# Performance work log

Measured on AMD Instinct MI355X. Metric: run time of the kernel, lower is better.

## Reference

```python
import jax, jax.numpy as jnp
import numpy as np

BATCH = 8192
IN_DIM = 512
OUT_DIM = 512
GRID_SIZE = 5
SPLINE_ORDER = 3
# grid has 2*(G+K)+1 knots -> after K de Boor steps basis count = 2*G+K
N_BASES = 2 * GRID_SIZE + SPLINE_ORDER  # 13
CLAMP_EPS = 1e-4
DENOM_EPS = 1e-8


def _make_grid():
    step = 2.0 / GRID_SIZE
    g = jnp.arange(-GRID_SIZE - SPLINE_ORDER, GRID_SIZE + SPLINE_ORDER + 1, dtype=jnp.float32) * step
    return jnp.tile(g[None, :], (IN_DIM, 1))  # [in_dim, 2*(G+K)+1]


def _b_spline(x, grid):
    # x: [B, in], grid: [in, L] -> bases: [B, in, 2*G+K]
    xg = x[..., None]  # [B, in, 1]
    bases = ((xg >= grid[:, :-1]) & (xg < grid[:, 1:])).astype(x.dtype)
    for k in range(1, SPLINE_ORDER + 1):
        denom1 = grid[:, k:-1] - grid[:, :-(k + 1)] + DENOM_EPS
        left = (xg - grid[:, :-(k + 1)]) / denom1
        denom2 = grid[:, k + 1:] - grid[:, 1:-k] + DENOM_EPS
        right = (grid[:, k + 1:] - xg) / denom2
        bases = left * bases[..., :-1] + right * bases[..., 1:]
    return bases


def setup_inputs() -> dict:
    key = jax.random.key(0)
    k1, k2, k3 = jax.random.split(key, 3)
    x = jax.random.normal(k1, (BATCH, IN_DIM), dtype=jnp.float32)
    # kaiming_uniform(a=sqrt(5)) ~ U(-1/sqrt(fan_in), 1/sqrt(fan_in))
    b_c = 1.0 / np.sqrt(IN_DIM * N_BASES)
    coeffs = jax.random.uniform(k2, (OUT_DIM, IN_DIM, N_BASES), dtype=jnp.float32, minval=-b_c, maxval=b_c)
    b_w = 1.0 / np.sqrt(IN_DIM)
    base_weight = jax.random.uniform(k3, (OUT_DIM, IN_DIM), dtype=jnp.float32, minval=-b_w, maxval=b_w)
    return {"x": x, "coeffs": coeffs, "base_weight": base_weight}


def reference(x, coeffs, base_weight):
    grid = _make_grid()
    xc = jnp.clip(x, -1.0 + CLAMP_EPS, 1.0 - CLAMP_EPS)
    basis = _b_spline(xc, grid)                       # [B, in, nb]
    spline_out = jnp.einsum('oic,bic->bo', coeffs, basis)
    base_out = jax.nn.silu(x) @ base_weight.T         # F.linear(silu(x), W)
    y = spline_out + base_out + x                     # residual (in_dim == out_dim)
    return y
```

## Files before the change

### kernel.cpp

```cpp
#include <hip/hip_runtime.h>
#include <stdint.h>

typedef unsigned int u32;
typedef unsigned short u16;
typedef unsigned long long u64;
typedef __bf16 bf16x8 __attribute__((ext_vector_type(8)));
typedef float f32x4 __attribute__((ext_vector_type(4)));
typedef u32 u32x4 __attribute__((ext_vector_type(4)));

#define IN_DIM 512

__device__ __forceinline__ u16 bfr(float f) {
  __bf16 h = (__bf16)f;
  return __builtin_bit_cast(u16, h);
}
__device__ __forceinline__ u16 f2bf(float f) {
  u32 u = __builtin_bit_cast(u32, f);
  u += 0x7fffu + ((u >> 16) & 1u);
  return (u16)(u >> 16);
}
__device__ __forceinline__ u32 pk2(float a, float b) {
  return (u32)f2bf(a) | ((u32)f2bf(b) << 16);
}

__global__ void pack_b(const float* __restrict__ coeffs,
                       const float* __restrict__ bw,
                       char* __restrict__ Bp) {
  __shared__ float stage[64][56];
  const int tid = threadIdx.x;
  const int q = tid & 3, g = tid >> 2;
  const int id = blockIdx.x * 64 + g;
  const int col = id >> 7, s = id & 127;
  const float* cbase = coeffs + ((size_t)col * IN_DIM + s * 4) * 13;
#pragma unroll
  for (int j = 0; j < 3; ++j) {
    int ch = q + j * 4;
    float4 v = *(const float4*)(cbase + ch * 4);
    stage[g][ch * 4 + 0] = v.x; stage[g][ch * 4 + 1] = v.y;
    stage[g][ch * 4 + 2] = v.z; stage[g][ch * 4 + 3] = v.w;
  }
  if (q == 0) {
    float4 v = *(const float4*)(cbase + 48);
    stage[g][48] = v.x; stage[g][49] = v.y; stage[g][50] = v.z; stage[g][51] = v.w;
  }
  if (q == 1) {
    float4 v = *(const float4*)(bw + (size_t)col * IN_DIM + s * 4);
    stage[g][52] = v.x; stage[g][53] = v.y; stage[g][54] = v.z; stage[g][55] = v.w;
  }
  __syncthreads();
  const int nbp = col >> 7, cb = (col >> 4) & 7, cl = col & 15;
  char* base = Bp + (((size_t)(nbp * 128 + s) * 8 + cb) * 2) * 1024;
#pragma unroll
  for (int r = 0; r < 2; ++r) {
    int idx = q * 2 + r;
    int h = idx & 1;
    int dd = idx >> 1;
    int ks = dd >> 1;
    const float* sf = &stage[g][dd * 13];
    float w = stage[g][52 + dd];
    u16 hh[8];
#pragma unroll
    for (int c = 0; c < 8; ++c) {
      int slot = h * 8 + c;
      float v = slot < 13 ? sf[slot] : (slot < 15 ? w : 0.0f);
      hh[c] = bfr(v);
    }
    u32x4 o;
    o.x = (u32)hh[0] | ((u32)hh[1] << 16);
    o.y = (u32)hh[2] | ((u32)hh[3] << 16);
    o.z = (u32)hh[4] | ((u32)hh[5] << 16);
    o.w = (u32)hh[6] | ((u32)hh[7] << 16);
    int lanei = cl + 16 * (2 * (dd & 1) + h);
    *(u32x4*)(base + (size_t)ks * 1024 + lanei * 16) = o;
  }
}

__device__ __forceinline__ void expandA(float xv, char* rb, u32 swz, u32 k0) {
  float xc = fminf(fmaxf(xv, -0.9999f), 0.9999f);
  float tp = __fmaf_rn(xc, 2.5f, 3.0f);
  float fj = floorf(tp);
  int jl = (int)fj;
  float u = tp - fj;
  float u2 = u * u, u3 = u2 * u;
  float vv = 1.0f - u;
  float b0 = vv * vv * vv * (1.0f / 6.0f);
  float b3 = u3 * (1.0f / 6.0f);
  float b1 = __fmaf_rn(0.5f, u3, __fmaf_rn(u2, -1.0f, 2.0f / 3.0f));
  float b2 = 1.0f - b0 - b1 - b3;
  float e = __expf(-xv);
  float sg = __fdividef(xv, 1.0f + e);
  u16 sh = bfr(sg);
  float shf = __builtin_bit_cast(float, ((u32)sh) << 16);
  u16 sl = bfr(sg - shf);
  u32 pk01 = (u32)bfr(b0) | ((u32)bfr(b1) << 16);
  u32 pk23 = (u32)bfr(b2) | ((u32)bfr(b3) << 16);
  u64 v = (u64)pk01 | (((u64)pk23) << 32);
  int sstart = jl + 2;
  int qa = sstart >> 2;
  int shn = (sstart & 3) << 4;
  u64 lo = v << shn;
  u64 hi = shn ? (v >> (64 - shn)) : 0ull;
  u64 q0 = qa ? 0ull : lo;
  u64 q1 = qa ? lo : hi;
  u64 q2 = qa ? hi : 0ull;
  u64 q3 = (u64)(((u32)sh) << 16) | (((u64)(u32)sl) << 32);
  u32x4 c0, c1;
  c0.x = (u32)q0; c0.y = (u32)(q0 >> 32); c0.z = (u32)q1; c0.w = (u32)(q1 >> 32);
  c1.x = (u32)q2; c1.y = (u32)(q2 >> 32); c1.z = (u32)q3; c1.w = (u32)(q3 >> 32);
  *(u32x4*)(rb + ((k0 ^ swz) << 4)) = c0;
  *(u32x4*)(rb + (((k0 + 1u) ^ swz) << 4)) = c1;
}

__launch_bounds__(768, 3)
__global__ void kan_gemm(const float* __restrict__ x,
                         const char* __restrict__ Bp,
                         float* __restrict__ out) {
  __shared__ __align__(16) char smem[67584];

  const int tid = threadIdx.x;
  const int lane = tid & 63;
  const int wid = tid >> 6;
  const bool isC = (wid < 8);

  const int kt = wid >> 2;
  const int wm = (wid >> 1) & 1, wn = wid & 1;
  const int lrow = lane & 15, lkg = lane >> 4;

  int s0 = blockIdx.x;
  int xcd = s0 & 7;
  int nb = xcd >> 1;
  int mb = ((s0 >> 3) << 1) | (xcd & 1);

  const int te = tid & 255;
  const int erow = te >> 2;
  const int ad = te & 3;
  const u32 aswz = (u32)(erow & 7);
  const u32 ak0 = (u32)(ad * 2);
  const float* xpa = x + (size_t)(mb * 128 + erow) * IN_DIM + ad;
  const float* xpb = xpa + (size_t)64 * IN_DIM;

  const char* bptr = Bp + (((size_t)(nb * 128) * 8 + wn * 4) * 2 + kt) * 1024 + (size_t)lane * 16;

  f32x4 acc[4][4];
#pragma unroll
  for (int i = 0; i < 4; ++i)
#pragma unroll
    for (int j = 0; j < 4; ++j) acc[i][j] = (f32x4){0.f, 0.f, 0.f, 0.f};

  u32x4 bA[4], bB[4];
  u32x4 afA[4], afB[4];
  char* r0 = smem;
  char* r1 = smem + 16384;
  char* r2 = smem + 32768;

  float xa1 = 0.f, xa2 = 0.f, xb1 = 0.f, xb2 = 0.f;
  if (isC) {
#pragma unroll
    for (int fn = 0; fn < 4; ++fn)
      bA[fn] = *(const u32x4*)(bptr + fn * 2048);
  } else {
    expandA(xpa[0], r0 + erow * 128, aswz, ak0);
    expandA(xpb[0], r0 + (erow + 64) * 128, aswz, ak0);
    expandA(xpa[4], r1 + erow * 128, aswz, ak0);
    expandA(xpb[4], r1 + (erow + 64) * 128, aswz, ak0);
    xa1 = xpa[8];  xb1 = xpb[8];
    xa2 = xpa[12]; xb2 = xpb[12];
  }
  __syncthreads();

  const u32 asl = (((u32)(kt * 4) | (u32)lkg) ^ (u32)(lrow & 7)) << 4;

  if (isC) {
    const char* arb0 = r0 + (wm * 64 + lrow) * 128;
#pragma unroll
    for (int fm = 0; fm < 4; ++fm)
      afA[fm] = *(const u32x4*)(arb0 + fm * 2048 + asl);
  }

#define STEP(S, RBN, WB, BCUR, BNXT, AFC, AFN)                                 \
  {                                                                            \
    if (isC) {                                                                 \
      const char* arbn = (RBN) + (wm * 64 + lrow) * 128;                       \
      _Pragma("unroll")                                                        \
      for (int fm = 0; fm < 4; ++fm)                                           \
        AFN[fm] = *(const u32x4*)(arbn + fm * 2048 + asl);                     \
      int sl_ = (S) + 1 < 128 ? (S) + 1 : 127;                                 \
      _Pragma("unroll")                                                        \
      for (int fn = 0; fn < 4; ++fn)                                           \
        BNXT[fn] = *(const u32x4*)(bptr + (size_t)sl_ * 16384 + fn * 2048);    \
      __builtin_amdgcn_s_setprio(1);                                           \
      _Pragma("unroll")                                                        \
      for (int fm = 0; fm < 4; ++fm)                                           \
        _Pragma("unroll")                                                      \
        for (int fn = 0; fn < 4; ++fn)                                         \
          acc[fm][fn] = __builtin_amdgcn_mfma_f32_16x16x32_bf16(               \
              __builtin_bit_cast(bf16x8, AFC[fm]),                             \
              __builtin_bit_cast(bf16x8, BCUR[fn]), acc[fm][fn], 0, 0, 0);     \
      __builtin_amdgcn_s_setprio(0);                                           \
    } else {                                                                   \
      if ((S) + 2 < 128) {                                                     \
        expandA(xa1, (WB) + erow * 128, aswz, ak0);                            \
        expandA(xb1, (WB) + (erow + 64) * 128, aswz, ak0);                     \
      }                                                                        \
      int xi = ((S) + 4 < 128 ? (S) + 4 : 127) * 4;                            \
      float na = xpa[xi], nbv = xpb[xi];                                       \
      xa1 = xa2; xa2 = na; xb1 = xb2; xb2 = nbv;                               \
      asm volatile("s_waitcnt lgkmcnt(0)" ::: "memory");                       \
    }                                                                          \
    __builtin_amdgcn_s_barrier();                                              \
  }

#pragma unroll 1
  for (int s = 0; s < 128; s += 2) {
    STEP(s, r1, r2, bA, bB, afA, afB)
    STEP(s + 1, r2, r0, bB, bA, afB, afA)
    char* t = r2; r2 = r1; r1 = r0; r0 = t;
  }

  __syncthreads();

  float* red = (float*)smem;
  if (isC && kt == 1) {
#pragma unroll
    for (int fm = 0; fm < 4; ++fm)
#pragma unroll
      for (int fn = 0; fn < 4; ++fn) {
        int rr = wm * 64 + fm * 16 + lkg * 4;
        int cc = wn * 64 + fn * 16 + lrow;
#pragma unroll
        for (int r = 0; r < 4; ++r)
          red[(size_t)(rr + r) * 132 + cc] = acc[fm][fn][r];
      }
  }
  __syncthreads();
  if (isC && kt == 0) {
#pragma unroll
    for (int fm = 0; fm < 4; ++fm)
#pragma unroll
      for (int fn = 0; fn < 4; ++fn) {
        int rr = wm * 64 + fm * 16 + lkg * 4;
        int cc = wn * 64 + fn * 16 + lrow;
        size_t gb = (size_t)(mb * 128 + rr) * IN_DIM + nb * 128 + cc;
#pragma unroll
        for (int r = 0; r < 4; ++r) {
          size_t off = gb + (size_t)r * IN_DIM;
          out[off] = acc[fm][fn][r] + red[(size_t)(rr + r) * 132 + cc] + x[off];
        }
      }
  }
}

__device__ __forceinline__ void st_b16(char* rb, u32 swz, u32 k0, int c, u16 v) {
  u32 uc = (u32)c;
  u32 byte = (((k0 + (uc >> 3)) ^ swz) << 4) | ((uc & 7u) << 1);
  *(u16*)(rb + byte) = v;
}

__device__ __forceinline__ void stage_a_fb(char* aT, int row, int d, float xv) {
  char* rb = aT + row * 128;
  u32 swz = (u32)(row & 7);
  float xc = fminf(fmaxf(xv, -0.9999f), 0.9999f);
  float tp = __fmaf_rn(xc, 2.5f, 3.0f);
  float fj = floorf(tp);
  int jl = (int)fj;
  float u = tp - fj;
  float u2 = u * u, u3 = u2 * u;
  float vv = 1.0f - u;
  float b0 = vv * vv * vv * (1.0f / 6.0f);
  float b3 = u3 * (1.0f / 6.0f);
  float b1 = __fmaf_rn(0.5f, u3, __fmaf_rn(u2, -1.0f, 2.0f / 3.0f));
  float b2 = 1.0f - b0 - b1 - b3;
  float e = __expf(-xv);
  float sg = __fdividef(xv, 1.0f + e);
  u16 sh = f2bf(sg);
  float shf = __builtin_bit_cast(float, ((u32)sh) << 16);
  u16 slo = f2bf(sg - shf);
  u32 k0 = (u32)d * 2u;
  u32x4 z = {0u, 0u, 0u, 0u};
  *(u32x4*)(rb + ((k0 ^ swz) << 4)) = z;
  u32x4 z2 = {0u, 0u, ((u32)sh) << 16, (u32)slo};
  *(u32x4*)(rb + (((k0 + 1u) ^ swz) << 4)) = z2;
  st_b16(rb, swz, k0, jl + 2, f2bf(b0));
  st_b16(rb, swz, k0, jl + 3, f2bf(b1));
  st_b16(rb, swz, k0, jl + 4, f2bf(b2));
  st_b16(rb, swz, k0, jl + 5, f2bf(b3));
}

__launch_bounds__(512, 2)
__global__ void kan_fused(const float* __restrict__ x,
                          const float* __restrict__ coeffs,
                          const float* __restrict__ bw,
                          float* __restrict__ out) {
  __shared__ __align__(16) char smem[65536];
  const int tid = threadIdx.x;
  const int lane = tid & 63;
  const int wid = tid >> 6;
  const int team = wid >> 2;
  const int wm = (wid >> 1) & 1;
  const int wn = wid & 1;
  const int m0 = wm * 64, n0 = wn * 64;
  const int lrow = lane & 15;
  const int lkg = lane >> 4;
  int s = blockIdx.x;
  int xcd = s & 7;
  int nb = xcd >> 1;
  int mb = (s >> 3) | ((xcd & 1) << 5);
  const int t = tid & 255;
  const int arow = t >> 1;
  const int h = t & 1;
  char* aT = smem + team * 16384;
  char* bT = smem + 32768 + team * 16384;
  const int dim0 = team * 256;
  const float* xptr = x + (size_t)(mb * 128 + arow) * IN_DIM + dim0 + 2 * h;
  const float* cptr = coeffs + ((size_t)((nb * 128 + arow) * IN_DIM) + dim0) * 13 + 26 * h;
  const float* wptr = bw + (size_t)(nb * 128 + arow) * IN_DIM + dim0 + 2 * h;
  f32x4 acc[4][4];
#pragma unroll
  for (int i = 0; i < 4; ++i)
#pragma unroll
    for (int j = 0; j < 4; ++j) acc[i][j] = (f32x4){0.f, 0.f, 0.f, 0.f};
  float2 xv, wv;
  float2 cv0, cv1, cv2, cv3, cv4, cv5, cv6, cv7, cv8, cv9, cv10, cv11, cv12;
#define PREFETCH(STP)                                                     \
  {                                                                       \
    const float* cp_ = cptr + (STP) * 52;                                 \
    xv = *(const float2*)(xptr + (STP) * 4);                              \
    wv = *(const float2*)(wptr + (STP) * 4);                              \
    cv0 = *(const float2*)(cp_ + 0);   cv1 = *(const float2*)(cp_ + 2);   \
    cv2 = *(const float2*)(cp_ + 4);   cv3 = *(const float2*)(cp_ + 6);   \
    cv4 = *(const float2*)(cp_ + 8);   cv5 = *(const float2*)(cp_ + 10);  \
    cv6 = *(const float2*)(cp_ + 12);  cv7 = *(const float2*)(cp_ + 14);  \
    cv8 = *(const float2*)(cp_ + 16);  cv9 = *(const float2*)(cp_ + 18);  \
    cv10 = *(const float2*)(cp_ + 20); cv11 = *(const float2*)(cp_ + 22); \
    cv12 = *(const float2*)(cp_ + 24);                                    \
  }
  PREFETCH(0)
  for (int st = 0; st < 64; ++st) {
    stage_a_fb(aT, arow, 2 * h + 0, xv.x);
    stage_a_fb(aT, arow, 2 * h + 1, xv.y);
    {
      char* rb = bT + arow * 128;
      u32 swz = (u32)(arow & 7);
      u32 k0 = (u32)(2 * h) * 2u;
      u32x4 lo, hi;
      lo.x = pk2(cv0.x, cv0.y); lo.y = pk2(cv1.x, cv1.y);
      lo.z = pk2(cv2.x, cv2.y); lo.w = pk2(cv3.x, cv3.y);
      hi.x = pk2(cv4.x, cv4.y); hi.y = pk2(cv5.x, cv5.y);
      {
        u16 wb = f2bf(wv.x);
        hi.z = (u32)f2bf(cv6.x) | ((u32)wb << 16);
        hi.w = (u32)wb;
      }
      *(u32x4*)(rb + ((k0 ^ swz) << 4)) = lo;
      *(u32x4*)(rb + (((k0 + 1u) ^ swz) << 4)) = hi;
      lo.x = pk2(cv6.y, cv7.x);  lo.y = pk2(cv7.y, cv8.x);
      lo.z = pk2(cv8.y, cv9.x);  lo.w = pk2(cv9.y, cv10.x);
      hi.x = pk2(cv10.y, cv11.x); hi.y = pk2(cv11.y, cv12.x);
      {
        u16 wb = f2bf(wv.y);
        hi.z = (u32)f2bf(cv12.y) | ((u32)wb << 16);
        hi.w = (u32)wb;
      }
      *(u32x4*)(rb + (((k0 + 2u) ^ swz) << 4)) = lo;
      *(u32x4*)(rb + (((k0 + 3u) ^ swz) << 4)) = hi;
    }
    __syncthreads();
    if (st != 63) { PREFETCH(st + 1) }
    {
      const char* arb = aT + (m0 + lrow) * 128;
      const char* brb = bT + (n0 + lrow) * 128;
      u32 rsw = (u32)(lrow & 7);
#pragma unroll
      for (int ks = 0; ks < 2; ++ks) {
        u32 sl2 = (((u32)(ks * 4) | (u32)lkg) ^ rsw) << 4;
        bf16x8 af[4], bfr2[4];
#pragma unroll
        for (int fm = 0; fm < 4; ++fm)
          af[fm] = __builtin_bit_cast(bf16x8, *(const u32x4*)(arb + fm * 2048 + sl2));
#pragma unroll
        for (int fn = 0; fn < 4; ++fn)
          bfr2[fn] = __builtin_bit_cast(bf16x8, *(const u32x4*)(brb + fn * 2048 + sl2));
#pragma unroll
        for (int fm = 0; fm < 4; ++fm)
#pragma unroll
          for (int fn = 0; fn < 4; ++fn)
            acc[fm][fn] = __builtin_amdgcn_mfma_f32_16x16x32_bf16(
                af[fm], bfr2[fn], acc[fm][fn], 0, 0, 0);
      }
    }
    __syncthreads();
  }
  float* red = (float*)smem;
  if (team == 1) {
#pragma unroll
    for (int fm = 0; fm < 4; ++fm)
#pragma unroll
      for (int fn = 0; fn < 4; ++fn) {
        int rr = m0 + fm * 16 + lkg * 4;
        int cc = n0 + fn * 16 + lrow;
#pragma unroll
        for (int r = 0; r < 4; ++r) red[(rr + r) * 128 + cc] = acc[fm][fn][r];
      }
  }
  __syncthreads();
  if (team == 0) {
#pragma unroll
    for (int fm = 0; fm < 4; ++fm)
#pragma unroll
      for (int fn = 0; fn < 4; ++fn) {
        int rr = m0 + fm * 16 + lkg * 4;
        int ccol = n0 + fn * 16 + lrow;
        int grow = mb * 128 + rr;
        int gcol = nb * 128 + ccol;
#pragma unroll
        for (int r = 0; r < 4; ++r) {
          float v = acc[fm][fn][r] + red[(rr + r) * 128 + ccol] +
                    x[(size_t)(grow + r) * IN_DIM + gcol];
          out[(size_t)(grow + r) * IN_DIM + gcol] = v;
        }
      }
  }
}

extern "C" void kernel_launch(void* const* d_in, const int* in_sizes, int n_in,
                              void* d_out, int out_size, void* d_ws, size_t ws_size,
                              hipStream_t stream) {
  const float* x = (const float*)d_in[0];
  const float* coeffs = (const float*)d_in[1];
  const float* bw = (const float*)d_in[2];
  float* out = (float*)d_out;
  if (ws_size >= (size_t)512 * 16384) {
    char* Bp = (char*)d_ws;
    hipLaunchKernelGGL(pack_b, dim3(1024), dim3(256), 0, stream, coeffs, bw, Bp);
    hipLaunchKernelGGL(kan_gemm, dim3(256), dim3(768), 0, stream, x, Bp, out);
  } else {
    hipLaunchKernelGGL(kan_fused, dim3(256), dim3(512), 0, stream, x, coeffs, bw, out);
  }
}
```

Baseline: 99.45 us.

## Batch four K-steps per barrier with double-buffered 64KB A-tile stages

The A-operand pipeline moves from a triple-buffered scheme with one barrier per K-step to a double-buffered scheme. Each stage holds four K-steps, so a barrier is needed only every four steps. Producer waves now expand four x columns per iteration and prefetch eight values two stages ahead. Consumer waves interleave A fragment loads, B register prefetch and MFMA blocks inside each stage. Shared memory per block grows from about 66KB to 128KB, which likely cuts resident blocks per CU and reduces latency hiding in exchange for fewer barriers.

```diff
diff --git a/kernel.cpp b/kernel.cpp
--- a/kernel.cpp
+++ b/kernel.cpp
@@ -111,11 +111,24 @@
   *(u32x4*)(rb + (((k0 + 1u) ^ swz) << 4)) = c1;
 }
 
+#define MM(AF, BV)                                                             \
+  {                                                                            \
+    __builtin_amdgcn_s_setprio(1);                                             \
+    _Pragma("unroll")                                                          \
+    for (int fm = 0; fm < 4; ++fm)                                             \
+      _Pragma("unroll")                                                        \
+      for (int fn = 0; fn < 4; ++fn)                                           \
+        acc[fm][fn] = __builtin_amdgcn_mfma_f32_16x16x32_bf16(                 \
+            __builtin_bit_cast(bf16x8, AF[fm]),                                \
+            __builtin_bit_cast(bf16x8, BV[fn]), acc[fm][fn], 0, 0, 0);         \
+    __builtin_amdgcn_s_setprio(0);                                             \
+  }
+
 __launch_bounds__(768, 3)
 __global__ void kan_gemm(const float* __restrict__ x,
                          const char* __restrict__ Bp,
                          float* __restrict__ out) {
-  __shared__ __align__(16) char smem[67584];
+  __shared__ __align__(16) char smem[131072];
 
   const int tid = threadIdx.x;
   const int lane = tid & 63;
@@ -148,73 +161,94 @@
     for (int j = 0; j < 4; ++j) acc[i][j] = (f32x4){0.f, 0.f, 0.f, 0.f};
 
   u32x4 bA[4], bB[4];
-  u32x4 afA[4], afB[4];
-  char* r0 = smem;
-  char* r1 = smem + 16384;
-  char* r2 = smem + 32768;
-
-  float xa1 = 0.f, xa2 = 0.f, xb1 = 0.f, xb2 = 0.f;
+  char* ab0 = smem;
+  char* ab1 = smem + 65536;
+
+  float xc[8];
+#pragma unroll
+  for (int j = 0; j < 8; ++j) xc[j] = 0.f;
+
   if (isC) {
 #pragma unroll
     for (int fn = 0; fn < 4; ++fn)
       bA[fn] = *(const u32x4*)(bptr + fn * 2048);
   } else {
-    expandA(xpa[0], r0 + erow * 128, aswz, ak0);
-    expandA(xpb[0], r0 + (erow + 64) * 128, aswz, ak0);
-    expandA(xpa[4], r1 + erow * 128, aswz, ak0);
-    expandA(xpb[4], r1 + (erow + 64) * 128, aswz, ak0);
-    xa1 = xpa[8];  xb1 = xpb[8];
-    xa2 = xpa[12]; xb2 = xpb[12];
+    float xi[8];
+#pragma unroll
+    for (int k = 0; k < 4; ++k) { xi[2 * k] = xpa[4 * k]; xi[2 * k + 1] = xpb[4 * k]; }
+#pragma unroll
+    for (int k = 0; k < 4; ++k) {
+      expandA(xi[2 * k],     ab0 + k * 16384 + erow * 128, aswz, ak0);
+      expandA(xi[2 * k + 1], ab0 + k * 16384 + (erow + 64) * 128, aswz, ak0);
+    }
+#pragma unroll
+    for (int k = 0; k < 4; ++k) { xc[2 * k] = xpa[16 + 4 * k]; xc[2 * k + 1] = xpb[16 + 4 * k]; }
   }
   __syncthreads();
 
   const u32 asl = (((u32)(kt * 4) | (u32)lkg) ^ (u32)(lrow & 7)) << 4;
 
-  if (isC) {
-    const char* arb0 = r0 + (wm * 64 + lrow) * 128;
-#pragma unroll
-    for (int fm = 0; fm < 4; ++fm)
-      afA[fm] = *(const u32x4*)(arb0 + fm * 2048 + asl);
-  }
-
-#define STEP(S, RBN, WB, BCUR, BNXT, AFC, AFN)                                 \
-  {                                                                            \
-    if (isC) {                                                                 \
-      const char* arbn = (RBN) + (wm * 64 + lrow) * 128;                       \
-      _Pragma("unroll")                                                        \
-      for (int fm = 0; fm < 4; ++fm)                                           \
-        AFN[fm] = *(const u32x4*)(arbn + fm * 2048 + asl);                     \
-      int sl_ = (S) + 1 < 128 ? (S) + 1 : 127;                                 \
-      _Pragma("unroll")                                                        \
-      for (int fn = 0; fn < 4; ++fn)                                           \
-        BNXT[fn] = *(const u32x4*)(bptr + (size_t)sl_ * 16384 + fn * 2048);    \
-      __builtin_amdgcn_s_setprio(1);                                           \
-      _Pragma("unroll")                                                        \
-      for (int fm = 0; fm < 4; ++fm)                                           \
-        _Pragma("unroll")                                                      \
-        for (int fn = 0; fn < 4; ++fn)                                         \
-          acc[fm][fn] = __builtin_amdgcn_mfma_f32_16x16x32_bf16(               \
-              __builtin_bit_cast(bf16x8, AFC[fm]),                             \
-              __builtin_bit_cast(bf16x8, BCUR[fn]), acc[fm][fn], 0, 0, 0);     \
-      __builtin_amdgcn_s_setprio(0);                                           \
-    } else {                                                                   \
-      if ((S) + 2 < 128) {                                                     \
-        expandA(xa1, (WB) + erow * 128, aswz, ak0);                            \
-        expandA(xb1, (WB) + (erow + 64) * 128, aswz, ak0);                     \
-      }                                                                        \
-      int xi = ((S) + 4 < 128 ? (S) + 4 : 127) * 4;                            \
-      float na = xpa[xi], nbv = xpb[xi];                                       \
-      xa1 = xa2; xa2 = na; xb1 = xb2; xb2 = nbv;                               \
-      asm volatile("s_waitcnt lgkmcnt(0)" ::: "memory");                       \
-    }                                                                          \
-    __builtin_amdgcn_s_barrier();                                              \
-  }
-
 #pragma unroll 1
-  for (int s = 0; s < 128; s += 2) {
-    STEP(s, r1, r2, bA, bB, afA, afB)
-    STEP(s + 1, r2, r0, bB, bA, afB, afA)
-    char* t = r2; r2 = r1; r1 = r0; r0 = t;
+  for (int iv = 0; iv < 32; ++iv) {
+    if (isC) {
+      const char* rb = (iv & 1) ? ab1 : ab0;
+      const char* arb = rb + (wm * 64 + lrow) * 128;
+      const int S = iv * 4;
+      u32x4 af0[4], af1[4];
+#pragma unroll
+      for (int fm = 0; fm < 4; ++fm)
+        af0[fm] = *(const u32x4*)(arb + fm * 2048 + asl);
+#pragma unroll
+      for (int fm = 0; fm < 4; ++fm)
+        af1[fm] = *(const u32x4*)(arb + 16384 + fm * 2048 + asl);
+#pragma unroll
+      for (int fn = 0; fn < 4; ++fn)
+        bB[fn] = *(const u32x4*)(bptr + (size_t)(S + 1) * 16384 + fn * 2048);
+      MM(af0, bA)
+#pragma unroll
+      for (int fm = 0; fm < 4; ++fm)
+        af0[fm] = *(const u32x4*)(arb + 2 * 16384 + fm * 2048 + asl);
+#pragma unroll
+      for (int fn = 0; fn < 4; ++fn)
+        bA[fn] = *(const u32x4*)(bptr + (size_t)(S + 2) * 16384 + fn * 2048);
+      MM(af1, bB)
+#pragma unroll
+      for (int fm = 0; fm < 4; ++fm)
+        af1[fm] = *(const u32x4*)(arb + 3 * 16384 + fm * 2048 + asl);
+#pragma unroll
+      for (int fn = 0; fn < 4; ++fn)
+        bB[fn] = *(const u32x4*)(bptr + (size_t)(S + 3) * 16384 + fn * 2048);
+      MM(af0, bA)
+      {
+        int sn = (S + 4 < 128) ? (S + 4) : 127;
+#pragma unroll
+        for (int fn = 0; fn < 4; ++fn)
+          bA[fn] = *(const u32x4*)(bptr + (size_t)sn * 16384 + fn * 2048);
+      }
+      MM(af1, bB)
+    } else {
+      if (iv + 1 < 32) {
+        char* wb = (iv & 1) ? ab0 : ab1;
+#pragma unroll
+        for (int k = 0; k < 4; ++k) {
+          expandA(xc[2 * k],     wb + k * 16384 + erow * 128, aswz, ak0);
+          expandA(xc[2 * k + 1], wb + k * 16384 + (erow + 64) * 128, aswz, ak0);
+        }
+      }
+      {
+        int v2 = (iv + 2 < 32) ? (iv + 2) : 31;
+        float xn[8];
+#pragma unroll
+        for (int k = 0; k < 4; ++k) {
+          xn[2 * k]     = xpa[v2 * 16 + 4 * k];
+          xn[2 * k + 1] = xpb[v2 * 16 + 4 * k];
+        }
+#pragma unroll
+        for (int j = 0; j < 8; ++j) xc[j] = xn[j];
+      }
+      asm volatile("s_waitcnt lgkmcnt(0)" ::: "memory");
+    }
+    __builtin_amdgcn_s_barrier();
   }
 
   __syncthreads();
```

Measured after the change: 89.21 us (median of 2 runs). 1.11x faster.
